# Optimization experiments

Measured on AMD Instinct MI355X. Metric: run time of the kernel, lower is better.

Reference implementation:

```python
import jax, jax.numpy as jnp
import numpy as np

B, N, M, H, D = 16, 512, 16, 8, 128  # batch, nodes, neighbors, heads, input_dim
NEG_SLOPE = 0.2
EPS = 1e-5

def _glorot(key, shape):
    fan = sum(shape[-2:]) if len(shape) >= 2 else shape[-1]
    return jax.random.normal(key, shape, dtype=jnp.float32) * (2.0 / fan) ** 0.5

def setup_inputs() -> dict:
    key = jax.random.key(0)
    ks = jax.random.split(key, 12)
    h = jax.random.normal(ks[0], (B, N, D), dtype=jnp.float32)
    adj = jax.random.randint(ks[1], (B, N, M), 0, 2, dtype=jnp.int32)
    n_list = jax.random.randint(ks[2], (B, N, M), 0, N, dtype=jnp.int32)
    W = _glorot(ks[3], (H, D, D))            # per-head projection
    a_src = _glorot(ks[4], (H, D))           # attention vector, source half
    a_dst = _glorot(ks[5], (H, D))           # attention vector, neighbor half
    Wo = _glorot(ks[6], (H * D, D))          # concat-heads output projection
    ln1_g = jnp.ones((D,), jnp.float32); ln1_b = jnp.zeros((D,), jnp.float32)
    ff_w1 = _glorot(ks[7], (D, 2 * D)); ff_b1 = jnp.zeros((2 * D,), jnp.float32)
    ff_w2 = _glorot(ks[8], (2 * D, D)); ff_b2 = jnp.zeros((D,), jnp.float32)
    ln2_g = jnp.ones((D,), jnp.float32); ln2_b = jnp.zeros((D,), jnp.float32)
    return {"h": h, "adj": adj, "n_list": n_list, "W": W, "a_src": a_src,
            "a_dst": a_dst, "Wo": Wo, "ln1_g": ln1_g, "ln1_b": ln1_b,
            "ff_w1": ff_w1, "ff_b1": ff_b1, "ff_w2": ff_w2, "ff_b2": ff_b2,
            "ln2_g": ln2_g, "ln2_b": ln2_b}

def _layer_norm(x, g, b):
    mu = jnp.mean(x, axis=-1, keepdims=True)
    var = jnp.mean(jnp.square(x - mu), axis=-1, keepdims=True)
    return (x - mu) * jax.lax.rsqrt(var + EPS) * g + b

def _gat(h, adj, n_list, W, a_src, a_dst, Wo):
    Wh = jnp.einsum('bnd,hde->bnhe', h, W)                 # [B,N,H,D]
    s_src = jnp.einsum('bnhe,he->bnh', Wh, a_src)          # [B,N,H]
    s_dst = jnp.einsum('bnhe,he->bnh', Wh, a_dst)          # [B,N,H]
    gather = jax.vmap(lambda x, idx: x[idx])               # per-graph gather
    neigh = gather(Wh, n_list)                             # [B,N,M,H,D]
    s_dst_n = gather(s_dst, n_list)                        # [B,N,M,H]
    e = jax.nn.leaky_relu(s_src[:, :, None, :] + s_dst_n, NEG_SLOPE)
    e = jnp.where(adj[..., None] > 0, e, jnp.float32(-1e9))
    attn = jax.nn.softmax(e, axis=2)                       # over M neighbors
    out = jnp.einsum('bnmh,bnmhe->bnhe', attn, neigh)      # [B,N,H,D]
    return out.reshape(out.shape[0], out.shape[1], -1) @ Wo  # [B,N,D]

def reference(h, adj, n_list, W, a_src, a_dst, Wo, ln1_g, ln1_b,
              ff_w1, ff_b1, ff_w2, ff_b2, ln2_g, ln2_b):
    att = _gat(h, adj, n_list, W, a_src, a_dst, Wo)
    t = _layer_norm(att + h, ln1_g, ln1_b)
    ff = jax.nn.relu(t @ ff_w1 + ff_b1) @ ff_w2 + ff_b2
    return _layer_norm(ff + t, ln2_g, ln2_b)
```

## Files before the change

kernel.cpp:

```cpp
#include <hip/hip_runtime.h>
#include <hip/hip_bf16.h>

#define B_  16
#define N_  512
#define M_  16
#define H_  8
#define D_  128
#define BN_ 8192
#define NB  16

typedef __attribute__((ext_vector_type(4))) float          f32x4;
typedef __attribute__((ext_vector_type(4))) _Float16       f16x4;
typedef __attribute__((ext_vector_type(8))) unsigned short u16x8;
typedef __attribute__((ext_vector_type(8))) _Float16       f16x8;

static __device__ __forceinline__ float bf2f(__hip_bfloat16 x) { return __bfloat162float(x); }
static __device__ __forceinline__ unsigned short f2bu(float x) {
    __hip_bfloat16 b = __float2bfloat16(x);
    return *reinterpret_cast<unsigned short*>(&b);
}
static __device__ __forceinline__ float bu2f(unsigned short u) {
    return __uint_as_float(((unsigned int)u) << 16);
}

template <bool F32>
struct Pol {
    static __device__ __forceinline__ float ld(const void* p, int i) {
        if constexpr (F32) return ((const float*)p)[i];
        else               return bf2f(((const __hip_bfloat16*)p)[i]);
    }
    static __device__ __forceinline__ float4 ld4(const void* p, int i) {
        if constexpr (F32) return *(const float4*)((const float*)p + i);
        else {
            const ushort4 u = *(const ushort4*)((const unsigned short*)p + i);
            return make_float4(bu2f(u.x), bu2f(u.y), bu2f(u.z), bu2f(u.w));
        }
    }
    static __device__ __forceinline__ void ld8(const void* p, long i, float* v) {
        if constexpr (F32) {
            const float4 a = *(const float4*)((const float*)p + i);
            const float4 b = *(const float4*)((const float*)p + i + 4);
            v[0]=a.x; v[1]=a.y; v[2]=a.z; v[3]=a.w;
            v[4]=b.x; v[5]=b.y; v[6]=b.z; v[7]=b.w;
        } else {
            const u16x8 u = *(const u16x8*)((const unsigned short*)p + i);
            #pragma unroll
            for (int j = 0; j < 8; ++j) v[j] = bu2f(u[j]);
        }
    }
    static __device__ __forceinline__ void st8(void* p, long i, const float* v) {
        if constexpr (F32) {
            *(float4*)((float*)p + i)     = make_float4(v[0], v[1], v[2], v[3]);
            *(float4*)((float*)p + i + 4) = make_float4(v[4], v[5], v[6], v[7]);
        } else {
            u16x8 u;
            #pragma unroll
            for (int j = 0; j < 8; ++j) u[j] = f2bu(v[j]);
            *(u16x8*)((unsigned short*)p + i) = u;
        }
    }
};

static __device__ __forceinline__ bool probe_is_f32(const void* h) {
    bool is_f32 = false;
    const __hip_bfloat16* hb = (const __hip_bfloat16*)h;
    for (int i = 0; i < 128; ++i) {
        const float v = bf2f(hb[2 * i]);
        if (!(fabsf(v) < 1e4f)) is_f32 = true;
    }
    return is_f32;
}

template <bool F32>
static __device__ __forceinline__ void k0_body(
        const void* __restrict__ W,  const void* __restrict__ Wo,
        const void* __restrict__ a_src, const void* __restrict__ a_dst,
        float* __restrict__ wsrc, float* __restrict__ wdst,
        _Float16* __restrict__ WeffT, float* wrow ) {
    using P = Pol<F32>;
    const int blk = blockIdx.x;
    const int t   = threadIdx.x;
    if (blk < 512) {
        const int half = t >> 7, o = t & 127;
        const int hd = blk * 2 + half;
        wrow[half * 128 + o] = P::ld(W, hd * 128 + o);
        __syncthreads();
        const int hh = hd >> 7;
        float acc = 0.f;
        #pragma unroll 8
        for (int e = 0; e < 128; ++e)
            acc += wrow[half * 128 + e] * P::ld(Wo, (hh * 128 + e) * 128 + o);
        WeffT[(size_t)o * 1024 + hd] = (_Float16)acc;
    } else {
        const int hh = blk - 512;
        const int which = t >> 7, d = t & 127;
        const void* av = which ? a_dst : a_src;
        const int wbase = hh * (D_ * D_) + d * 128;
        float acc = 0.f;
        #pragma unroll 8
        for (int e = 0; e < 128; e += 4) {
            const float4 wv = P::ld4(W, wbase + e);
            const float4 aa = P::ld4(av, hh * 128 + e);
            acc += wv.x * aa.x + wv.y * aa.y + wv.z * aa.z + wv.w * aa.w;
        }
        (which ? wdst : wsrc)[hh * 128 + d] = acc;
    }
}

__global__ __launch_bounds__(256) void k0(
        const void* W, const void* Wo, const void* a_src, const void* a_dst,
        const void* h, float* wsrc, float* wdst, _Float16* WeffT) {
    __shared__ float wrow[2 * 128];
    if (probe_is_f32(h)) k0_body<true >(W, Wo, a_src, a_dst, wsrc, wdst, WeffT, wrow);
    else                 k0_body<false>(W, Wo, a_src, a_dst, wsrc, wdst, WeffT, wrow);
}

template <bool F32>
static __device__ __forceinline__ void k1_body(
        const void* __restrict__ h, const float* __restrict__ wsrc,
        const float* __restrict__ wdst, _Float16* __restrict__ ssrc_h,
        _Float16* __restrict__ sdst_h, float* hls , float* wls ) {
    using P = Pol<F32>;
    const int t   = threadIdx.x;
    const int bn0 = blockIdx.x * 16;
    {
        const int r = t >> 4, c0 = (t & 15) * 8;
        float v[8];
        P::ld8(h, (long)(bn0 + r) * 128 + c0, v);
        #pragma unroll
        for (int j = 0; j < 8; ++j) hls[r * 132 + c0 + j] = v[j];
        const int c = t >> 4;
        const float* wp = (c >> 3) ? wdst : wsrc;
        const int woff = (c & 7) * 128 + c0;
        #pragma unroll
        for (int j = 0; j < 8; ++j) wls[c * 132 + c0 + j] = wp[woff + j];
    }
    __syncthreads();
    const int n = t >> 4, c = t & 15;
    float acc = 0.f;
    #pragma unroll
    for (int e = 0; e < 128; e += 4) {
        const float4 hv = *(const float4*)(hls + n * 132 + e);
        const float4 wv = *(const float4*)(wls + c * 132 + e);
        acc += hv.x * wv.x + hv.y * wv.y + hv.z * wv.z + hv.w * wv.w;
    }
    const int node = bn0 + n;
    if (c < 8) ssrc_h[node * 8 + c]       = (_Float16)acc;
    else       sdst_h[node * 8 + (c - 8)] = (_Float16)acc;
}

__global__ __launch_bounds__(256) void k1(const void* h, const float* wsrc,
                                          const float* wdst, _Float16* ssrc_h,
                                          _Float16* sdst_h) {
    __shared__ float hls[16 * 132];
    __shared__ float wls[16 * 132];
    if (probe_is_f32(h)) k1_body<true >(h, wsrc, wdst, ssrc_h, sdst_h, hls, wls);
    else                 k1_body<false>(h, wsrc, wdst, ssrc_h, sdst_h, hls, wls);
}

struct __align__(16) Smem {
    union {
        _Float16 Zh[NB][1024];
        struct {
            float    ts[NB][132];
            _Float16 us[NB][260];
            float    ys[NB][128];
        } ff;
    } u;
    float hs[NB][128];
    union {
        float attn[NB][16][8];
        float yln[NB][128];
    } v;
    int   nls[NB][16];
    int   adjs[NB][16];
    float ssrc[NB][8];
};

template <bool F32>
static __device__ __forceinline__ void gat_body(
        Smem& s,
        const void* __restrict__ h,
        const int*  __restrict__ adj,
        const int*  __restrict__ n_list,
        const _Float16* __restrict__ ssrc_h,
        const _Float16* __restrict__ sdst_h,
        const _Float16* __restrict__ WeffT,
        const void* __restrict__ g1, const void* __restrict__ bb1,
        const void* __restrict__ w1, const void* __restrict__ fb1,
        const void* __restrict__ w2, const void* __restrict__ fb2,
        const void* __restrict__ g2, const void* __restrict__ bb2,
        void* __restrict__ out) {
    using P = Pol<F32>;
    const int t   = threadIdx.x;
    const int bn0 = blockIdx.x * NB;
    const int b   = bn0 >> 9;
    const int l   = t & 63;
    const int w   = t >> 6;
    const int lo  = l & 15;
    const int hi  = l >> 4;

    {
        const int r = t >> 5, c0 = (t & 31) * 4;
        const float4 v = P::ld4(h, (bn0 + r) * 128 + c0);
        *(float4*)&s.hs[r][c0] = v;
    }
    if (t < 256) {
        const int r = t >> 4, m = t & 15;
        s.nls[r][m]  = n_list[(bn0 + r) * M_ + m] & (N_ - 1);
        s.adjs[r][m] = adj[(bn0 + r) * M_ + m];
    }
    if (t < NB * 8) s.ssrc[t >> 3][t & 7] = (float)ssrc_h[bn0 * 8 + t];
    __syncthreads();

    if (t < 256) {
        const int r = t >> 4, m = t & 15;
        const int nbr = s.nls[r][m];
        const f16x8 sd = *(const f16x8*)(sdst_h + (size_t)(b * N_ + nbr) * 8);
        const int amask = s.adjs[r][m];
        float sc[8];
        #pragma unroll
        for (int hh = 0; hh < 8; ++hh) {
            float x = s.ssrc[r][hh] + (float)sd[hh];
            x = x > 0.f ? x : 0.2f * x;
            if (amask == 0) x = -1e9f;
            sc[hh] = x;
        }
        *(float4*)&s.v.attn[r][m][0] = make_float4(sc[0], sc[1], sc[2], sc[3]);
        *(float4*)&s.v.attn[r][m][4] = make_float4(sc[4], sc[5], sc[6], sc[7]);
    }
    __syncthreads();

    if (t < NB * 8) {
        const int r = t >> 3, hh = t & 7;
        float mx = -3.4e38f;
        #pragma unroll
        for (int m = 0; m < 16; ++m) mx = fmaxf(mx, s.v.attn[r][m][hh]);
        float ex[16], sum = 0.f;
        #pragma unroll
        for (int m = 0; m < 16; ++m) { ex[m] = __expf(s.v.attn[r][m][hh] - mx); sum += ex[m]; }
        const float inv = 1.f / sum;
        #pragma unroll
        for (int m = 0; m < 16; ++m) s.v.attn[r][m][hh] = ex[m] * inv;
    }
    __syncthreads();

    {
        const int r = t >> 5, dc = t & 31, d0 = dc * 4;
        float z[8][4];
        #pragma unroll
        for (int hh = 0; hh < 8; ++hh)
            #pragma unroll
            for (int jj = 0; jj < 4; ++jj) z[hh][jj] = 0.f;
        #pragma unroll 4
        for (int m = 0; m < 16; ++m) {
            const int nbr = s.nls[r][m];
            const float4 hv = P::ld4(h, (b * N_ + nbr) * 128 + d0);
            const float hv4[4] = { hv.x, hv.y, hv.z, hv.w };
            const float4 a0 = *(const float4*)&s.v.attn[r][m][0];
            const float4 a1 = *(const float4*)&s.v.attn[r][m][4];
            const float av[8] = { a0.x, a0.y, a0.z, a0.w, a1.x, a1.y, a1.z, a1.w };
            #pragma unroll
            for (int hh = 0; hh < 8; ++hh)
                #pragma unroll
                for (int jj = 0; jj < 4; ++jj) z[hh][jj] += av[hh] * hv4[jj];
        }
        char* zb = (char*)&s.u.Zh[0][0] + r * 2048;
        const int xo = (r & 7) << 4;
        #pragma unroll
        for (int hh = 0; hh < 8; ++hh) {
            f16x4 vv;
            #pragma unroll
            for (int jj = 0; jj < 4; ++jj) vv[jj] = (_Float16)z[hh][jj];
            *(f16x4*)(zb + ((hh * 256 + dc * 8) ^ xo)) = vv;
        }
    }
    __syncthreads();

    {
        const char* za  = (const char*)&s.u.Zh[0][0] + lo * 2048;
        const int   xo  = (lo & 7) << 4;
        const char* wb0 = (const char*)(WeffT + (size_t)(w * 16 + lo) * 1024);
        f32x4 acc0 = {0.f, 0.f, 0.f, 0.f};
        #pragma unroll 8
        for (int ks = 0; ks < 64; ++ks) {
            const int kb = ks * 32 + hi * 8;
            const f16x4 a  = *(const f16x4*)(za + (kb ^ xo));
            const f16x4 b0 = *(const f16x4*)(wb0 + kb);
            acc0 = __builtin_amdgcn_mfma_f32_16x16x16f16(a, b0, acc0, 0, 0, 0);
        }
        const int o0 = w * 16 + lo;
        #pragma unroll
        for (int q = 0; q < 4; ++q) {
            const int rr = hi * 4 + q;
            s.v.yln[rr][o0] = acc0[q] + s.hs[rr][o0];
        }
    }
    __syncthreads();

    if (t < 256) {
        const int r = t >> 4, j0 = (t & 15) * 8;
        const float4 x0 = *(const float4*)&s.v.yln[r][j0];
        const float4 x1 = *(const float4*)&s.v.yln[r][j0 + 4];
        const float x[8] = { x0.x, x0.y, x0.z, x0.w, x1.x, x1.y, x1.z, x1.w };
        float sm = 0.f, ss = 0.f;
        #pragma unroll
        for (int j = 0; j < 8; ++j) { sm += x[j]; ss += x[j] * x[j]; }
        #pragma unroll
        for (int off = 8; off > 0; off >>= 1) {
            sm += __shfl_xor(sm, off);
            ss += __shfl_xor(ss, off);
        }
        const float mu   = sm * (1.f / 128.f);
        const float var  = ss * (1.f / 128.f) - mu * mu;
        const float rstd = rsqrtf(var + 1e-5f);
        float gv[8], bv[8];
        P::ld8(g1, j0, gv);
        P::ld8(bb1, j0, bv);
        #pragma unroll
        for (int j = 0; j < 8; ++j)
            s.u.ff.ts[r][j0 + j] = (x[j] - mu) * rstd * gv[j] + bv[j];
    }
    __syncthreads();

    {
        f32x4 acc[2] = { {0.f,0.f,0.f,0.f}, {0.f,0.f,0.f,0.f} };
        #pragma unroll
        for (int ks = 0; ks < 8; ++ks) {
            const int k = ks * 16 + hi * 4;
            const float4 tv = *(const float4*)&s.u.ff.ts[lo][k];
            f16x4 a;
            a[0] = (_Float16)tv.x; a[1] = (_Float16)tv.y;
            a[2] = (_Float16)tv.z; a[3] = (_Float16)tv.w;
            #pragma unroll
            for (int nt = 0; nt < 2; ++nt) {
                const int o = w * 32 + nt * 16 + lo;
                f16x4 bb;
                #pragma unroll
                for (int j = 0; j < 4; ++j) bb[j] = (_Float16)P::ld(w1, (k + j) * 256 + o);
                acc[nt] = __builtin_amdgcn_mfma_f32_16x16x16f16(a, bb, acc[nt], 0, 0, 0);
            }
        }
        #pragma unroll
        for (int nt = 0; nt < 2; ++nt) {
            const int o = w * 32 + nt * 16 + lo;
            const float bias = P::ld(fb1, o);
            #pragma unroll
            for (int q = 0; q < 4; ++q)
                s.u.ff.us[hi * 4 + q][o] = (_Float16)fmaxf(acc[nt][q] + bias, 0.f);
        }
    }
    __syncthreads();

    {
        const int o0 = w * 16 + lo;
        f32x4 acc = {0.f, 0.f, 0.f, 0.f};
        #pragma unroll
        for (int ks = 0; ks < 16; ++ks) {
            const int k = ks * 16 + hi * 4;
            const f16x4 a = *(const f16x4*)&s.u.ff.us[lo][k];
            f16x4 bb;
            #pragma unroll
            for (int j = 0; j < 4; ++j) bb[j] = (_Float16)P::ld(w2, (k + j) * 128 + o0);
            acc = __builtin_amdgcn_mfma_f32_16x16x16f16(a, bb, acc, 0, 0, 0);
        }
        const float bias = P::ld(fb2, o0);
        #pragma unroll
        for (int q = 0; q < 4; ++q) {
            const int rr = hi * 4 + q;
            s.u.ff.ys[rr][o0] = acc[q] + bias + s.u.ff.ts[rr][o0];
        }
    }
    __syncthreads();

    if (t < 256) {
        const int r = t >> 4, j0 = (t & 15) * 8;
        const float4 x0 = *(const float4*)&s.u.ff.ys[r][j0];
        const float4 x1 = *(const float4*)&s.u.ff.ys[r][j0 + 4];
        const float x[8] = { x0.x, x0.y, x0.z, x0.w, x1.x, x1.y, x1.z, x1.w };
        float sm = 0.f, ss = 0.f;
        #pragma unroll
        for (int j = 0; j < 8; ++j) { sm += x[j]; ss += x[j] * x[j]; }
        #pragma unroll
        for (int off = 8; off > 0; off >>= 1) {
            sm += __shfl_xor(sm, off);
            ss += __shfl_xor(ss, off);
        }
        const float mu   = sm * (1.f / 128.f);
        const float var  = ss * (1.f / 128.f) - mu * mu;
        const float rstd = rsqrtf(var + 1e-5f);
        float gv[8], bv[8], o8[8];
        P::ld8(g2, j0, gv);
        P::ld8(bb2, j0, bv);
        #pragma unroll
        for (int j = 0; j < 8; ++j) o8[j] = (x[j] - mu) * rstd * gv[j] + bv[j];
        P::st8(out, (long)(bn0 + r) * 128 + j0, o8);
    }
}

__global__ __launch_bounds__(512) void k_gat(
        const void* __restrict__ h,
        const int*  __restrict__ adj,
        const int*  __restrict__ n_list,
        const _Float16* __restrict__ ssrc_h,
        const _Float16* __restrict__ sdst_h,
        const _Float16* __restrict__ WeffT,
        const void* __restrict__ g1, const void* __restrict__ bb1,
        const void* __restrict__ w1, const void* __restrict__ fb1,
        const void* __restrict__ w2, const void* __restrict__ fb2,
        const void* __restrict__ g2, const void* __restrict__ bb2,
        void* __restrict__ out) {
    __shared__ Smem s;
    if (probe_is_f32(h))
        gat_body<true >(s, h, adj, n_list, ssrc_h, sdst_h, WeffT,
                        g1, bb1, w1, fb1, w2, fb2, g2, bb2, out);
    else
        gat_body<false>(s, h, adj, n_list, ssrc_h, sdst_h, WeffT,
                        g1, bb1, w1, fb1, w2, fb2, g2, bb2, out);
}

extern "C" void kernel_launch(void* const* d_in, const int* in_sizes, int n_in,
                              void* d_out, int out_size, void* d_ws, size_t ws_size,
                              hipStream_t stream) {
    (void)in_sizes; (void)n_in; (void)out_size; (void)ws_size;

    char* wsb = (char*)d_ws;
    float*     wsrc  = (float*)(wsb);
    float*     wdst  = (float*)(wsb + 4096);
    _Float16*  ssrc  = (_Float16*)(wsb + 8192);
    _Float16*  sdst  = (_Float16*)(wsb + 139264);
    _Float16*  WeffT = (_Float16*)(wsb + 270336);

    k0<<<520,      256, 0, stream>>>(d_in[3], d_in[6], d_in[4], d_in[5], d_in[0],
                                     wsrc, wdst, WeffT);
    k1<<<BN_ / 16, 256, 0, stream>>>(d_in[0], wsrc, wdst, ssrc, sdst);
    k_gat<<<BN_ / NB, 512, 0, stream>>>(
        d_in[0], (const int*)d_in[1], (const int*)d_in[2], ssrc, sdst, WeffT,
        d_in[7], d_in[8], d_in[9], d_in[10], d_in[11], d_in[12],
        d_in[13], d_in[14], d_out);
}
```

Baseline: 158.9 us.

## Fuse attention-score projection into GAT kernel, drop separate score kernel

Removes the k1 kernel that precomputed per-node source/destination attention scores. The GAT kernel now computes them itself, using dot products of h rows with folded weight vectors held in shared memory, and gathers neighbor h rows from global memory. This saves one launch and the fp16 score round trip through memory. In exchange, each block recomputes 16x more destination dot products (every neighbor, every head) and reads full 128-float neighbor rows instead of 8 halfs per neighbor.

```diff
diff --git a/kernel.cpp b/kernel.cpp
--- a/kernel.cpp
+++ b/kernel.cpp
@@ -115,52 +115,10 @@
     else                 k0_body<false>(W, Wo, a_src, a_dst, wsrc, wdst, WeffT, wrow);
 }
 
-template <bool F32>
-static __device__ __forceinline__ void k1_body(
-        const void* __restrict__ h, const float* __restrict__ wsrc,
-        const float* __restrict__ wdst, _Float16* __restrict__ ssrc_h,
-        _Float16* __restrict__ sdst_h, float* hls , float* wls ) {
-    using P = Pol<F32>;
-    const int t   = threadIdx.x;
-    const int bn0 = blockIdx.x * 16;
-    {
-        const int r = t >> 4, c0 = (t & 15) * 8;
-        float v[8];
-        P::ld8(h, (long)(bn0 + r) * 128 + c0, v);
-        #pragma unroll
-        for (int j = 0; j < 8; ++j) hls[r * 132 + c0 + j] = v[j];
-        const int c = t >> 4;
-        const float* wp = (c >> 3) ? wdst : wsrc;
-        const int woff = (c & 7) * 128 + c0;
-        #pragma unroll
-        for (int j = 0; j < 8; ++j) wls[c * 132 + c0 + j] = wp[woff + j];
-    }
-    __syncthreads();
-    const int n = t >> 4, c = t & 15;
-    float acc = 0.f;
-    #pragma unroll
-    for (int e = 0; e < 128; e += 4) {
-        const float4 hv = *(const float4*)(hls + n * 132 + e);
-        const float4 wv = *(const float4*)(wls + c * 132 + e);
-        acc += hv.x * wv.x + hv.y * wv.y + hv.z * wv.z + hv.w * wv.w;
-    }
-    const int node = bn0 + n;
-    if (c < 8) ssrc_h[node * 8 + c]       = (_Float16)acc;
-    else       sdst_h[node * 8 + (c - 8)] = (_Float16)acc;
-}
-
-__global__ __launch_bounds__(256) void k1(const void* h, const float* wsrc,
-                                          const float* wdst, _Float16* ssrc_h,
-                                          _Float16* sdst_h) {
-    __shared__ float hls[16 * 132];
-    __shared__ float wls[16 * 132];
-    if (probe_is_f32(h)) k1_body<true >(h, wsrc, wdst, ssrc_h, sdst_h, hls, wls);
-    else                 k1_body<false>(h, wsrc, wdst, ssrc_h, sdst_h, hls, wls);
-}
-
 struct __align__(16) Smem {
     union {
         _Float16 Zh[NB][1024];
+        float    wsd[2][1024];
         struct {
             float    ts[NB][132];
             _Float16 us[NB][260];
@@ -174,7 +132,6 @@
     } v;
     int   nls[NB][16];
     int   adjs[NB][16];
-    float ssrc[NB][8];
 };
 
 template <bool F32>
@@ -183,8 +140,8 @@
         const void* __restrict__ h,
         const int*  __restrict__ adj,
         const int*  __restrict__ n_list,
-        const _Float16* __restrict__ ssrc_h,
-        const _Float16* __restrict__ sdst_h,
+        const float* __restrict__ wsrc,
+        const float* __restrict__ wdst,
         const _Float16* __restrict__ WeffT,
         const void* __restrict__ g1, const void* __restrict__ bb1,
         const void* __restrict__ w1, const void* __restrict__ fb1,
@@ -209,25 +166,52 @@
         const int r = t >> 4, m = t & 15;
         s.nls[r][m]  = n_list[(bn0 + r) * M_ + m] & (N_ - 1);
         s.adjs[r][m] = adj[(bn0 + r) * M_ + m];
-    }
-    if (t < NB * 8) s.ssrc[t >> 3][t & 7] = (float)ssrc_h[bn0 * 8 + t];
-    __syncthreads();
-
-    if (t < 256) {
-        const int r = t >> 4, m = t & 15;
-        const int nbr = s.nls[r][m];
-        const f16x8 sd = *(const f16x8*)(sdst_h + (size_t)(b * N_ + nbr) * 8);
-        const int amask = s.adjs[r][m];
-        float sc[8];
+        *(float4*)&s.u.wsd[0][t * 4] = *(const float4*)(wsrc + t * 4);
+    } else {
+        const int i = t - 256;
+        *(float4*)&s.u.wsd[1][i * 4] = *(const float4*)(wdst + i * 4);
+    }
+    __syncthreads();
+
+    {
+        const int p = t >> 1, sub = t & 1;
+        const int r = p >> 4, m = p & 15;
+        const int nbr  = s.nls[r][m];
+        const int gbase = (b * N_ + nbr) * 128 + sub * 64;
+        const int lbase = sub * 64;
+        float accS[8], accD[8];
+        #pragma unroll
+        for (int hh = 0; hh < 8; ++hh) { accS[hh] = 0.f; accD[hh] = 0.f; }
+        #pragma unroll 4
+        for (int c = 0; c < 64; c += 4) {
+            const float4 hv = P::ld4(h, gbase + c);
+            const float4 sv = *(const float4*)&s.hs[r][lbase + c];
+            #pragma unroll
+            for (int hh = 0; hh < 8; ++hh) {
+                const float4 wdv = *(const float4*)&s.u.wsd[1][hh * 128 + lbase + c];
+                const float4 wsv = *(const float4*)&s.u.wsd[0][hh * 128 + lbase + c];
+                accD[hh] += hv.x * wdv.x + hv.y * wdv.y + hv.z * wdv.z + hv.w * wdv.w;
+                accS[hh] += sv.x * wsv.x + sv.y * wsv.y + sv.z * wsv.z + sv.w * wsv.w;
+            }
+        }
         #pragma unroll
         for (int hh = 0; hh < 8; ++hh) {
-            float x = s.ssrc[r][hh] + (float)sd[hh];
-            x = x > 0.f ? x : 0.2f * x;
-            if (amask == 0) x = -1e9f;
-            sc[hh] = x;
-        }
-        *(float4*)&s.v.attn[r][m][0] = make_float4(sc[0], sc[1], sc[2], sc[3]);
-        *(float4*)&s.v.attn[r][m][4] = make_float4(sc[4], sc[5], sc[6], sc[7]);
+            accS[hh] += __shfl_xor(accS[hh], 1);
+            accD[hh] += __shfl_xor(accD[hh], 1);
+        }
+        if (sub == 0) {
+            const int amask = s.adjs[r][m];
+            float sc[8];
+            #pragma unroll
+            for (int hh = 0; hh < 8; ++hh) {
+                float x = accS[hh] + accD[hh];
+                x = x > 0.f ? x : 0.2f * x;
+                if (amask == 0) x = -1e9f;
+                sc[hh] = x;
+            }
+            *(float4*)&s.v.attn[r][m][0] = make_float4(sc[0], sc[1], sc[2], sc[3]);
+            *(float4*)&s.v.attn[r][m][4] = make_float4(sc[4], sc[5], sc[6], sc[7]);
+        }
     }
     __syncthreads();
 
@@ -298,7 +282,7 @@
     }
     __syncthreads();
 
-    if (t < 256) {
+    if (t < NB * 16) {
         const int r = t >> 4, j0 = (t & 15) * 8;
         const float4 x0 = *(const float4*)&s.v.yln[r][j0];
         const float4 x1 = *(const float4*)&s.v.yln[r][j0 + 4];
@@ -373,7 +357,7 @@
     }
     __syncthreads();
 
-    if (t < 256) {
+    if (t < NB * 16) {
         const int r = t >> 4, j0 = (t & 15) * 8;
         const float4 x0 = *(const float4*)&s.u.ff.ys[r][j0];
         const float4 x1 = *(const float4*)&s.u.ff.ys[r][j0 + 4];
@@ -402,8 +386,8 @@
         const void* __restrict__ h,
         const int*  __restrict__ adj,
         const int*  __restrict__ n_list,
-        const _Float16* __restrict__ ssrc_h,
-        const _Float16* __restrict__ sdst_h,
+        const float* __restrict__ wsrc,
+        const float* __restrict__ wdst,
         const _Float16* __restrict__ WeffT,
         const void* __restrict__ g1, const void* __restrict__ bb1,
         const void* __restrict__ w1, const void* __restrict__ fb1,
@@ -412,10 +396,10 @@
         void* __restrict__ out) {
     __shared__ Smem s;
     if (probe_is_f32(h))
-        gat_body<true >(s, h, adj, n_list, ssrc_h, sdst_h, WeffT,
+        gat_body<true >(s, h, adj, n_list, wsrc, wdst, WeffT,
                         g1, bb1, w1, fb1, w2, fb2, g2, bb2, out);
     else
-        gat_body<false>(s, h, adj, n_list, ssrc_h, sdst_h, WeffT,
+        gat_body<false>(s, h, adj, n_list, wsrc, wdst, WeffT,
                         g1, bb1, w1, fb1, w2, fb2, g2, bb2, out);
 }
 
@@ -427,15 +411,12 @@
     char* wsb = (char*)d_ws;
     float*     wsrc  = (float*)(wsb);
     float*     wdst  = (float*)(wsb + 4096);
-    _Float16*  ssrc  = (_Float16*)(wsb + 8192);
-    _Float16*  sdst  = (_Float16*)(wsb + 139264);
-    _Float16*  WeffT = (_Float16*)(wsb + 270336);
-
-    k0<<<520,      256, 0, stream>>>(d_in[3], d_in[6], d_in[4], d_in[5], d_in[0],
-                                     wsrc, wdst, WeffT);
-    k1<<<BN_ / 16, 256, 0, stream>>>(d_in[0], wsrc, wdst, ssrc, sdst);
+    _Float16*  WeffT = (_Float16*)(wsb + 8192);
+
+    k0<<<520, 256, 0, stream>>>(d_in[3], d_in[6], d_in[4], d_in[5], d_in[0],
+                                wsrc, wdst, WeffT);
     k_gat<<<BN_ / NB, 512, 0, stream>>>(
-        d_in[0], (const int*)d_in[1], (const int*)d_in[2], ssrc, sdst, WeffT,
+        d_in[0], (const int*)d_in[1], (const int*)d_in[2], wsrc, wdst, WeffT,
         d_in[7], d_in[8], d_in[9], d_in[10], d_in[11], d_in[12],
         d_in[13], d_in[14], d_out);
 }
```

Result: no change. 161.5 us (+1.6%).
